# Kernel tuning notes

Hardware: AMD Instinct MI355X
Metric: run time of the kernel (lower is better)

## Reference

```python
import jax, jax.numpy as jnp
import numpy as np

E = 192      # embed_dim
DI = 384     # d_inner = 2*E (mamba default expand=2)
S = 16       # d_state
R = 12       # dt_rank = ceil(E/16)
DEPTH = 4
STRIDE = 4
P = 400      # num_patches = 1600/4
NC = 20
BATCH = 32
EPS = 1e-5


def _rmsnorm(x, w):
    x = x.astype(jnp.float32)
    return x * jax.lax.rsqrt(jnp.mean(x * x, axis=-1, keepdims=True) + EPS) * w


def _mamba_mixer(h, in_w, cw, cb, xpw, dtw, dtb, a_log, d_skip, ow):
    # h: [B, L, E]
    Bsz, Ln, _ = h.shape
    xz = jnp.einsum('ble,de->bld', h, in_w)            # [B,L,2*DI]
    xm, z = xz[..., :DI], xz[..., DI:]
    # causal depthwise conv1d, kernel 4 (left pad 3, truncate to L)
    xp = jnp.pad(xm, ((0, 0), (3, 0), (0, 0)))
    xc = sum(xp[:, k:k + Ln, :] * cw[:, k] for k in range(4)) + cb
    xc = jax.nn.silu(xc)
    xdb = jnp.einsum('bld,rd->blr', xc, xpw)           # [B,L,R+2S]
    dt = jax.nn.softplus(jnp.einsum('blr,dr->bld', xdb[..., :R], dtw) + dtb)
    Bm = xdb[..., R:R + S]
    Cm = xdb[..., R + S:]
    A = -jnp.exp(a_log)                                # [DI,S]

    def step(hst, inp):
        dt_t, b_t, c_t, u_t = inp                      # [B,DI],[B,S],[B,S],[B,DI]
        dA = jnp.exp(dt_t[:, :, None] * A)             # [B,DI,S]
        hst = dA * hst + (dt_t * u_t)[:, :, None] * b_t[:, None, :]
        y_t = jnp.einsum('bdn,bn->bd', hst, c_t)
        return hst, y_t

    h0 = jnp.zeros((Bsz, DI, S), xc.dtype)
    xs = (dt.transpose(1, 0, 2), Bm.transpose(1, 0, 2), Cm.transpose(1, 0, 2), xc.transpose(1, 0, 2))
    _, ys = jax.lax.scan(step, h0, xs)
    y = ys.transpose(1, 0, 2) + xc * d_skip
    y = y * jax.nn.silu(z)
    return jnp.einsum('bld,ed->ble', y, ow)


def _forward(imgs, patch_w, patch_b, cls_token, pos_embed, cnn_w, cnn_b, norm_w,
             in_proj_w, conv_w, conv_b, x_proj_w, dt_proj_w, dt_proj_b, A_log, D,
             out_proj_w, norm_f_w, head_w, head_b):
    Bsz = imgs.shape[0]
    # StrideEmbed: conv1d kernel=stride=4 == reshape + matmul
    x = imgs.reshape(Bsz, P, STRIDE)
    x = jnp.einsum('blk,ek->ble', x, patch_w[:, 0, :]) + patch_b   # [B,P,E]
    x = x + pos_embed[:, :-1, :]
    # depthwise conv1d k=3 pad=1 over length
    xp = jnp.pad(x, ((0, 0), (1, 1), (0, 0)))
    x = sum(xp[:, k:k + P, :] * cnn_w[:, 0, k] for k in range(3)) + cnn_b
    cls = cls_token + pos_embed[:, -1, :]                           # [1,1,E]
    x = jnp.concatenate([x, jnp.broadcast_to(cls, (Bsz, 1, E))], axis=1)  # [B,401,E]

    hidden = x
    residual = None
    for i in range(DEPTH):
        residual = hidden if residual is None else residual + hidden
        hn = _rmsnorm(residual, norm_w[i])
        hidden = _mamba_mixer(hn, in_proj_w[i], conv_w[i], conv_b[i], x_proj_w[i],
                              dt_proj_w[i], dt_proj_b[i], A_log[i], D[i], out_proj_w[i])
    out = _rmsnorm(hidden + residual, norm_f_w)
    v_sem = out[:, -1, :]
    return v_sem @ head_w.T + head_b


def setup_inputs() -> dict:
    key = jax.random.key(0)
    ks = jax.random.split(key, 12)
    n = lambda k, shp, s=0.02: jax.random.normal(k, shp, dtype=jnp.float32) * s
    return {
        'imgs': jax.random.normal(ks[0], (BATCH, 1, 40, 40), jnp.float32),
        'patch_w': n(ks[1], (E, 1, STRIDE), 0.3),
        'patch_b': jnp.zeros((E,), jnp.float32),
        'cls_token': n(ks[2], (1, 1, E)),
        'pos_embed': n(ks[3], (1, P + 1, E)),
        'cnn_w': n(ks[4], (E, 1, 3), 0.3),
        'cnn_b': jnp.zeros((E,), jnp.float32),
        'norm_w': jnp.ones((DEPTH, E), jnp.float32),
        'in_proj_w': n(ks[5], (DEPTH, 2 * DI, E), 0.05),
        'conv_w': n(ks[6], (DEPTH, DI, 4), 0.3),
        'conv_b': jnp.zeros((DEPTH, DI), jnp.float32),
        'x_proj_w': n(ks[7], (DEPTH, R + 2 * S, DI), 0.05),
        'dt_proj_w': n(ks[8], (DEPTH, DI, R), 0.3),
        'dt_proj_b': jnp.log(jnp.expm1(jax.random.uniform(ks[9], (DEPTH, DI), minval=0.001, maxval=0.1))),
        'A_log': jnp.log(jnp.broadcast_to(jnp.arange(1, S + 1, dtype=jnp.float32), (DEPTH, DI, S))),
        'D': jnp.ones((DEPTH, DI), jnp.float32),
        'out_proj_w': n(ks[10], (DEPTH, E, DI), 0.05),
        'norm_f_w': jnp.ones((E,), jnp.float32),
        'head_w': n(ks[11], (NC, E)),
        'head_b': jnp.zeros((NC,), jnp.float32),
    }


def reference(imgs, patch_w, patch_b, cls_token, pos_embed, cnn_w, cnn_b, norm_w,
              in_proj_w, conv_w, conv_b, x_proj_w, dt_proj_w, dt_proj_b, A_log, D,
              out_proj_w, norm_f_w, head_w, head_b):
    return _forward(imgs, patch_w, patch_b, cls_token, pos_embed, cnn_w, cnn_b, norm_w,
                    in_proj_w, conv_w, conv_b, x_proj_w, dt_proj_w, dt_proj_b, A_log, D,
                    out_proj_w, norm_f_w, head_w, head_b)
```

## Files before the change

kernel.cpp:

```cpp
#include <hip/hip_runtime.h>
#include <math.h>

#define E 192
#define DI 384
#define S 16
#define R 12
#define DEPTH 4
#define P 400
#define NC 20
#define BATCH 32
#define L 401
#define NTOK (BATCH * L)
#define CH 32
#define NCH 13

using short8 = __attribute__((ext_vector_type(8))) short;
using float4v = __attribute__((ext_vector_type(4))) float;

__device__ __forceinline__ float siluf(float x) {
    return x / (1.f + __expf(-x));
}
__device__ __forceinline__ float softplusf(float x) {
    return (x > 20.f) ? x : log1pf(__expf(x));
}
__device__ __forceinline__ unsigned short f2bf(float x) {
    unsigned int u = __float_as_uint(x);
    unsigned int r = 0x7fffu + ((u >> 16) & 1u);
    return (unsigned short)((u + r) >> 16);
}

__global__ void k_embed(const float* __restrict__ imgs, const float* __restrict__ patch_w,
                        const float* __restrict__ patch_b, const float* __restrict__ cls_token,
                        const float* __restrict__ pos_embed, const float* __restrict__ cnn_w,
                        const float* __restrict__ cnn_b, float* __restrict__ resid) {
    int idx = blockIdx.x * blockDim.x + threadIdx.x;
    if (idx >= NTOK * E) return;
    int e = idx % E;
    int bl = idx / E;
    int l = bl % L;
    int b = bl / L;
    float out;
    if (l == P) {
        out = cls_token[e] + pos_embed[(size_t)P * E + e];
    } else {
        float w0 = patch_w[e * 4 + 0], w1 = patch_w[e * 4 + 1];
        float w2 = patch_w[e * 4 + 2], w3 = patch_w[e * 4 + 3];
        float pb = patch_b[e];
        const float* ib = imgs + (size_t)b * 1600;
        auto xe = [&](int ll) -> float {
            const float* ip = ib + ll * 4;
            return ip[0] * w0 + ip[1] * w1 + ip[2] * w2 + ip[3] * w3 + pb +
                   pos_embed[(size_t)ll * E + e];
        };
        float c0 = cnn_w[e * 3 + 0], c1 = cnn_w[e * 3 + 1], c2 = cnn_w[e * 3 + 2];
        float acc = cnn_b[e] + xe(l) * c1;
        if (l > 0) acc += xe(l - 1) * c0;
        if (l < P - 1) acc += xe(l + 1) * c2;
        out = acc;
    }
    resid[idx] = out;
}

template <bool ADD>
__global__ void k_rmsnorm(const float* __restrict__ hidden, float* __restrict__ resid,
                          unsigned short* __restrict__ hn, const float* __restrict__ w) {
    int wave = blockIdx.x * (blockDim.x >> 6) + (threadIdx.x >> 6);
    int lane = threadIdx.x & 63;
    if (wave >= NTOK) return;
    size_t base = (size_t)wave * E;
    float v[3];
    float ss = 0.f;
#pragma unroll
    for (int j = 0; j < 3; j++) {
        int e = lane + j * 64;
        float r = resid[base + e];
        if (ADD) {
            r += hidden[base + e];
            resid[base + e] = r;
        }
        v[j] = r;
        ss += r * r;
    }
#pragma unroll
    for (int off = 32; off > 0; off >>= 1) ss += __shfl_xor(ss, off, 64);
    float scale = rsqrtf(ss * (1.f / (float)E) + 1e-5f);
#pragma unroll
    for (int j = 0; j < 3; j++) {
        int e = lane + j * 64;
        hn[base + e] = f2bf(v[j] * scale * w[e]);
    }
}

__global__ void k_cvt(const float* __restrict__ src, unsigned short* __restrict__ dst, int n) {
    int idx = blockIdx.x * blockDim.x + threadIdx.x;
    if (idx < n) dst[idx] = f2bf(src[idx]);
}

__global__ void k_preA(const float* __restrict__ A_log, float* __restrict__ negA, int n) {
    int idx = blockIdx.x * blockDim.x + threadIdx.x;
    if (idx < n) negA[idx] = -__expf(A_log[idx]);
}

template <int BM>
__global__ __launch_bounds__(256) void k_gemm_bf16(const unsigned short* __restrict__ A,
                                                   const unsigned short* __restrict__ W,
                                                   float* __restrict__ C, int M, int N, int K) {
    constexpr int BN = 64, BK = 64, PADK = BK + 8;
    constexpr int MT = BM / 32;
    __shared__ unsigned short As[BM][PADK];
    __shared__ unsigned short Bs[BN][PADK];
    int tid = threadIdx.x;
    int m0 = blockIdx.y * BM, n0 = blockIdx.x * BN;
    int wave = tid >> 6, lane = tid & 63;
    int row16 = lane & 15, quad = lane >> 4;
    int wm0 = (wave >> 1) * (BM / 2), wn0 = (wave & 1) * 32;

    float4v acc[MT][2];
#pragma unroll
    for (int i = 0; i < MT; i++)
#pragma unroll
        for (int j = 0; j < 2; j++) acc[i][j] = (float4v){0.f, 0.f, 0.f, 0.f};

    for (int k0 = 0; k0 < K; k0 += BK) {
#pragma unroll
        for (int p = 0; p < MT; p++) {
            int idx = (p * 256 + tid) * 8;
            int row = idx / BK, col = idx % BK;
            int gm = m0 + row;
            short8 v;
            if (gm < M)
                v = *(const short8*)&A[(size_t)gm * K + k0 + col];
            else
                v = (short8)0;
            *(short8*)&As[row][col] = v;
        }
#pragma unroll
        for (int p = 0; p < 2; p++) {
            int idx = (p * 256 + tid) * 8;
            int row = idx / BK, col = idx % BK;
            int gn = n0 + row;
            short8 v;
            if (gn < N)
                v = *(const short8*)&W[(size_t)gn * K + k0 + col];
            else
                v = (short8)0;
            *(short8*)&Bs[row][col] = v;
        }
        __syncthreads();
#pragma unroll
        for (int kk = 0; kk < BK; kk += 32) {
            int koff = kk + quad * 8;
            short8 af[MT], bfr[2];
#pragma unroll
            for (int i = 0; i < MT; i++)
                af[i] = *(const short8*)&As[wm0 + i * 16 + row16][koff];
#pragma unroll
            for (int j = 0; j < 2; j++)
                bfr[j] = *(const short8*)&Bs[wn0 + j * 16 + row16][koff];
#pragma unroll
            for (int i = 0; i < MT; i++)
#pragma unroll
                for (int j = 0; j < 2; j++)
                    acc[i][j] = __builtin_amdgcn_mfma_f32_16x16x32_bf16(af[i], bfr[j],
                                                                        acc[i][j], 0, 0, 0);
        }
        __syncthreads();
    }
#pragma unroll
    for (int i = 0; i < MT; i++) {
#pragma unroll
        for (int j = 0; j < 2; j++) {
#pragma unroll
            for (int r = 0; r < 4; r++) {
                int m = m0 + wm0 + i * 16 + quad * 4 + r;
                int n = n0 + wn0 + j * 16 + row16;
                if (m < M && n < N) C[(size_t)m * N + n] = acc[i][j][r];
            }
        }
    }
}

__global__ void k_conv(const float* __restrict__ xz, const float* __restrict__ cw,
                       const float* __restrict__ cb, float* __restrict__ xc,
                       unsigned short* __restrict__ xc_bf) {
    int idx = blockIdx.x * blockDim.x + threadIdx.x;
    if (idx >= NTOK * DI) return;
    int d = idx % DI;
    int bl = idx / DI;
    int l = bl % L;
    int b = bl / L;
    const float* base = xz + (size_t)b * L * (2 * DI) + d;
    float acc = cb[d];
#pragma unroll
    for (int k = 0; k < 4; k++) {
        int ll = l - 3 + k;
        if (ll >= 0) acc += base[(size_t)ll * (2 * DI)] * cw[d * 4 + k];
    }
    float v = siluf(acc);
    xc[idx] = v;
    xc_bf[idx] = f2bf(v);
}

__global__ void k_scanA(const float* __restrict__ xc, const float* __restrict__ xdb,
                        const float* __restrict__ negA, const float* __restrict__ dtw,
                        const float* __restrict__ dtb, const float* __restrict__ Dskip,
                        float* __restrict__ ylocal, float* __restrict__ dtcum,
                        float* __restrict__ hend) {
    int d = threadIdx.x;
    int ch = blockIdx.x;
    int b = blockIdx.y;
    int t0 = ch * CH;
    int t1 = min(t0 + CH, L);
    float a[S];
#pragma unroll
    for (int n = 0; n < S; n++) a[n] = negA[d * S + n];
    float wdt[R];
#pragma unroll
    for (int r = 0; r < R; r++) wdt[r] = dtw[d * R + r];
    float bias = dtb[d];
    float dsk = Dskip[d];
    float h[S] = {};
    float dts = 0.f;
    for (int t = t0; t < t1; t++) {
        size_t tok = (size_t)b * L + t;
        const float* row = xdb + tok * 44;
        float dtacc = bias;
#pragma unroll
        for (int r = 0; r < R; r++) dtacc += row[r] * wdt[r];
        float dtv = softplusf(dtacc);
        dts += dtv;
        float u = xc[tok * DI + d];
        float dtu = dtv * u;
        float y = u * dsk;
#pragma unroll
        for (int n = 0; n < S; n++) {
            float dA = __expf(dtv * a[n]);
            h[n] = dA * h[n] + dtu * row[R + n];
            y += h[n] * row[R + S + n];
        }
        ylocal[tok * DI + d] = y;
        dtcum[tok * DI + d] = dts;
    }
    size_t o = (((size_t)b * NCH + ch) * DI + d) * S;
#pragma unroll
    for (int n = 0; n < S; n++) hend[o + n] = h[n];
}

__global__ void k_scanB(const float* __restrict__ hend, const float* __restrict__ dtcum,
                        const float* __restrict__ negA, float* __restrict__ hinit) {
    int idx = blockIdx.x * blockDim.x + threadIdx.x;
    if (idx >= BATCH * DI) return;
    int d = idx % DI;
    int b = idx / DI;
    float a[S];
#pragma unroll
    for (int n = 0; n < S; n++) a[n] = negA[d * S + n];
    float h[S] = {};
    for (int ch = 0; ch < NCH; ch++) {
        size_t o = (((size_t)b * NCH + ch) * DI + d) * S;
#pragma unroll
        for (int n = 0; n < S; n++) hinit[o + n] = h[n];
        int tlast = min(ch * CH + CH, L) - 1;
        float dts = dtcum[((size_t)b * L + tlast) * DI + d];
#pragma unroll
        for (int n = 0; n < S; n++) h[n] = __expf(dts * a[n]) * h[n] + hend[o + n];
    }
}

__global__ void k_fixup(const float* __restrict__ xz, const float* __restrict__ xdb,
                        const float* __restrict__ negA, const float* __restrict__ hinit,
                        const float* __restrict__ ylocal, const float* __restrict__ dtcum,
                        unsigned short* __restrict__ y_bf) {
    int idx = blockIdx.x * blockDim.x + threadIdx.x;
    if (idx >= NTOK * DI) return;
    int d = idx % DI;
    int tok = idx / DI;
    int l = tok % L;
    int b = tok / L;
    int ch = l / CH;
    float y = ylocal[idx];
    if (ch != 0) {
        float dts = dtcum[idx];
        const float* h0 = hinit + (((size_t)b * NCH + ch) * DI + d) * S;
        const float* an = negA + d * S;
        const float* cv = xdb + (size_t)tok * 44 + R + S;
        float corr = 0.f;
#pragma unroll
        for (int n = 0; n < S; n++) corr += cv[n] * __expf(an[n] * dts) * h0[n];
        y += corr;
    }
    float z = xz[(size_t)tok * (2 * DI) + DI + d];
    y_bf[idx] = f2bf(y * siluf(z));
}

__global__ void k_head(const float* __restrict__ resid, const float* __restrict__ hidden,
                       const float* __restrict__ norm_f_w, const float* __restrict__ head_w,
                       const float* __restrict__ head_b, float* __restrict__ out) {
    __shared__ float v[E];
    int b = blockIdx.x;
    int lane = threadIdx.x;
    size_t base = ((size_t)b * L + P) * E;
    float loc[3];
    float ss = 0.f;
#pragma unroll
    for (int j = 0; j < 3; j++) {
        int e = lane + j * 64;
        float x = resid[base + e] + hidden[base + e];
        loc[j] = x;
        ss += x * x;
    }
#pragma unroll
    for (int off = 32; off > 0; off >>= 1) ss += __shfl_xor(ss, off, 64);
    float scale = rsqrtf(ss * (1.f / (float)E) + 1e-5f);
#pragma unroll
    for (int j = 0; j < 3; j++) {
        int e = lane + j * 64;
        v[e] = loc[j] * scale * norm_f_w[e];
    }
    __syncthreads();
    if (lane < NC) {
        float acc = head_b[lane];
        for (int e = 0; e < E; e++) acc += v[e] * head_w[lane * E + e];
        out[b * NC + lane] = acc;
    }
}

extern "C" void kernel_launch(void* const* d_in, const int* in_sizes, int n_in,
                              void* d_out, int out_size, void* d_ws, size_t ws_size,
                              hipStream_t stream) {
    const float* imgs      = (const float*)d_in[0];
    const float* patch_w   = (const float*)d_in[1];
    const float* patch_b   = (const float*)d_in[2];
    const float* cls_token = (const float*)d_in[3];
    const float* pos_embed = (const float*)d_in[4];
    const float* cnn_w     = (const float*)d_in[5];
    const float* cnn_b     = (const float*)d_in[6];
    const float* norm_w    = (const float*)d_in[7];
    const float* in_proj_w = (const float*)d_in[8];
    const float* conv_w    = (const float*)d_in[9];
    const float* conv_b    = (const float*)d_in[10];
    const float* x_proj_w  = (const float*)d_in[11];
    const float* dt_proj_w = (const float*)d_in[12];
    const float* dt_proj_b = (const float*)d_in[13];
    const float* A_log     = (const float*)d_in[14];
    const float* Dskip     = (const float*)d_in[15];
    const float* out_proj_w= (const float*)d_in[16];
    const float* norm_f_w  = (const float*)d_in[17];
    const float* head_w    = (const float*)d_in[18];
    const float* head_b    = (const float*)d_in[19];

    float* ws = (float*)d_ws;
    size_t off = 0;
    float* resid  = ws + off; off += (size_t)NTOK * E;
    float* hidden = ws + off; off += (size_t)NTOK * E;
    float* xz     = ws + off; off += (size_t)NTOK * 2 * DI;
    float* xc     = ws + off; off += (size_t)NTOK * DI;
    float* xdb    = ws + off; off += (size_t)NTOK * 44;
    float* ylocal = ws + off; off += (size_t)NTOK * DI;
    float* dtcum  = ws + off; off += (size_t)NTOK * DI;
    float* hend   = ws + off; off += (size_t)BATCH * NCH * DI * S;
    float* hinit  = ws + off; off += (size_t)BATCH * NCH * DI * S;
    float* negA   = ws + off; off += (size_t)DEPTH * DI * S;
    unsigned short* bf_buf = (unsigned short*)(ws + off); off += (size_t)NTOK * DI / 2;
    unsigned short* w_in  = (unsigned short*)(ws + off); off += (size_t)DEPTH * 2 * DI * E / 2;
    unsigned short* w_x   = (unsigned short*)(ws + off); off += (size_t)DEPTH * 44 * DI / 2 + 16;
    unsigned short* w_out = (unsigned short*)(ws + off); off += (size_t)DEPTH * E * DI / 2;

    unsigned short* hn_bf = bf_buf;
    unsigned short* xc_bf = bf_buf;
    unsigned short* y_bf  = bf_buf;

    {
        int n1 = DEPTH * 2 * DI * E;
        k_cvt<<<(n1 + 255) / 256, 256, 0, stream>>>(in_proj_w, w_in, n1);
        int n2 = DEPTH * 44 * DI;
        k_cvt<<<(n2 + 255) / 256, 256, 0, stream>>>(x_proj_w, w_x, n2);
        int n3 = DEPTH * E * DI;
        k_cvt<<<(n3 + 255) / 256, 256, 0, stream>>>(out_proj_w, w_out, n3);
        int n4 = DEPTH * DI * S;
        k_preA<<<(n4 + 255) / 256, 256, 0, stream>>>(A_log, negA, n4);
    }

    k_embed<<<(NTOK * E) / 256, 256, 0, stream>>>(imgs, patch_w, patch_b, cls_token,
                                                  pos_embed, cnn_w, cnn_b, resid);

    for (int i = 0; i < DEPTH; i++) {
        if (i == 0)
            k_rmsnorm<false><<<NTOK / 4, 256, 0, stream>>>(hidden, resid, hn_bf, norm_w + i * E);
        else
            k_rmsnorm<true><<<NTOK / 4, 256, 0, stream>>>(hidden, resid, hn_bf, norm_w + i * E);

        {
            dim3 g((2 * DI) / 64, (NTOK + 127) / 128);
            k_gemm_bf16<128><<<g, 256, 0, stream>>>(hn_bf, w_in + (size_t)i * 2 * DI * E, xz,
                                                    NTOK, 2 * DI, E);
        }
        k_conv<<<(NTOK * DI) / 256, 256, 0, stream>>>(xz, conv_w + (size_t)i * DI * 4,
                                                      conv_b + (size_t)i * DI, xc, xc_bf);
        {
            dim3 g(1, NTOK / 32);
            k_gemm_bf16<32><<<g, 256, 0, stream>>>(xc_bf, w_x + (size_t)i * 44 * DI, xdb,
                                                   NTOK, 44, DI);
        }
        {
            const float* nA = negA + (size_t)i * DI * S;
            dim3 g(NCH, BATCH);
            k_scanA<<<g, DI, 0, stream>>>(xc, xdb, nA, dt_proj_w + (size_t)i * DI * R,
                                          dt_proj_b + (size_t)i * DI, Dskip + (size_t)i * DI,
                                          ylocal, dtcum, hend);
            k_scanB<<<(BATCH * DI + 255) / 256, 256, 0, stream>>>(hend, dtcum, nA, hinit);
            k_fixup<<<(NTOK * DI + 255) / 256, 256, 0, stream>>>(xz, xdb, nA, hinit,
                                                                 ylocal, dtcum, y_bf);
        }
        {
            dim3 g(E / 64, (NTOK + 63) / 64);
            k_gemm_bf16<64><<<g, 256, 0, stream>>>(y_bf, w_out + (size_t)i * E * DI, hidden,
                                                   NTOK, E, DI);
        }
    }

    k_head<<<BATCH, 64, 0, stream>>>(resid, hidden, norm_f_w, head_w, head_b, (float*)d_out);
}
```

Before: 877.4 us.

## Split scan state across thread pairs, halve chunk size, retile GEMMs, fuse prep kernels

The chunked selective scan now gives each (d) channel two threads, each owning half of the 16 state entries. The two halves of y are combined with a lane shuffle, and the chunk length drops from 32 to 16, which doubles the number of chunks. The GEMM template gains a BN parameter: the in_proj GEMM uses 128x128 tiles and the out_proj GEMM uses 128x64 tiles. The four weight-prep launches are merged into one kernel. The scan changes aim to raise parallelism and shorten the serial dependency chain, at the cost of redundant dt computation per thread pair and larger hend/hinit buffers plus more scanB serial work.

```diff
diff --git a/kernel.cpp b/kernel.cpp
--- a/kernel.cpp
+++ b/kernel.cpp
@@ -11,8 +11,8 @@
 #define BATCH 32
 #define L 401
 #define NTOK (BATCH * L)
-#define CH 32
-#define NCH 13
+#define CH 16
+#define NCH 26
 
 using short8 = __attribute__((ext_vector_type(8))) short;
 using float4v = __attribute__((ext_vector_type(4))) float;
@@ -91,35 +91,48 @@
     }
 }
 
-__global__ void k_cvt(const float* __restrict__ src, unsigned short* __restrict__ dst, int n) {
+__global__ void k_prep(const float* __restrict__ in_proj_w, const float* __restrict__ x_proj_w,
+                       const float* __restrict__ out_proj_w, const float* __restrict__ A_log,
+                       unsigned short* __restrict__ w_in, unsigned short* __restrict__ w_x,
+                       unsigned short* __restrict__ w_out, float* __restrict__ negA) {
+    const int n1 = DEPTH * 2 * DI * E;
+    const int n2 = DEPTH * 44 * DI;
+    const int n3 = DEPTH * E * DI;
+    const int n4 = DEPTH * DI * S;
     int idx = blockIdx.x * blockDim.x + threadIdx.x;
-    if (idx < n) dst[idx] = f2bf(src[idx]);
-}
-
-__global__ void k_preA(const float* __restrict__ A_log, float* __restrict__ negA, int n) {
-    int idx = blockIdx.x * blockDim.x + threadIdx.x;
-    if (idx < n) negA[idx] = -__expf(A_log[idx]);
-}
-
-template <int BM>
+    if (idx < n1) {
+        w_in[idx] = f2bf(in_proj_w[idx]);
+    } else if (idx < n1 + n2) {
+        int i = idx - n1;
+        w_x[i] = f2bf(x_proj_w[i]);
+    } else if (idx < n1 + n2 + n3) {
+        int i = idx - n1 - n2;
+        w_out[i] = f2bf(out_proj_w[i]);
+    } else if (idx < n1 + n2 + n3 + n4) {
+        int i = idx - n1 - n2 - n3;
+        negA[i] = -__expf(A_log[i]);
+    }
+}
+
+template <int BM, int BN>
 __global__ __launch_bounds__(256) void k_gemm_bf16(const unsigned short* __restrict__ A,
                                                    const unsigned short* __restrict__ W,
                                                    float* __restrict__ C, int M, int N, int K) {
-    constexpr int BN = 64, BK = 64, PADK = BK + 8;
-    constexpr int MT = BM / 32;
+    constexpr int BK = 64, PADK = BK + 8;
+    constexpr int MT = BM / 32, NT = BN / 32;
     __shared__ unsigned short As[BM][PADK];
     __shared__ unsigned short Bs[BN][PADK];
     int tid = threadIdx.x;
     int m0 = blockIdx.y * BM, n0 = blockIdx.x * BN;
     int wave = tid >> 6, lane = tid & 63;
     int row16 = lane & 15, quad = lane >> 4;
-    int wm0 = (wave >> 1) * (BM / 2), wn0 = (wave & 1) * 32;
-
-    float4v acc[MT][2];
+    int wm0 = (wave >> 1) * (BM / 2), wn0 = (wave & 1) * (BN / 2);
+
+    float4v acc[MT][NT];
 #pragma unroll
     for (int i = 0; i < MT; i++)
 #pragma unroll
-        for (int j = 0; j < 2; j++) acc[i][j] = (float4v){0.f, 0.f, 0.f, 0.f};
+        for (int j = 0; j < NT; j++) acc[i][j] = (float4v){0.f, 0.f, 0.f, 0.f};
 
     for (int k0 = 0; k0 < K; k0 += BK) {
 #pragma unroll
@@ -135,7 +148,7 @@
             *(short8*)&As[row][col] = v;
         }
 #pragma unroll
-        for (int p = 0; p < 2; p++) {
+        for (int p = 0; p < NT; p++) {
             int idx = (p * 256 + tid) * 8;
             int row = idx / BK, col = idx % BK;
             int gn = n0 + row;
@@ -150,17 +163,17 @@
 #pragma unroll
         for (int kk = 0; kk < BK; kk += 32) {
             int koff = kk + quad * 8;
-            short8 af[MT], bfr[2];
+            short8 af[MT], bfr[NT];
 #pragma unroll
             for (int i = 0; i < MT; i++)
                 af[i] = *(const short8*)&As[wm0 + i * 16 + row16][koff];
 #pragma unroll
-            for (int j = 0; j < 2; j++)
+            for (int j = 0; j < NT; j++)
                 bfr[j] = *(const short8*)&Bs[wn0 + j * 16 + row16][koff];
 #pragma unroll
             for (int i = 0; i < MT; i++)
 #pragma unroll
-                for (int j = 0; j < 2; j++)
+                for (int j = 0; j < NT; j++)
                     acc[i][j] = __builtin_amdgcn_mfma_f32_16x16x32_bf16(af[i], bfr[j],
                                                                         acc[i][j], 0, 0, 0);
         }
@@ -169,7 +182,7 @@
 #pragma unroll
     for (int i = 0; i < MT; i++) {
 #pragma unroll
-        for (int j = 0; j < 2; j++) {
+        for (int j = 0; j < NT; j++) {
 #pragma unroll
             for (int r = 0; r < 4; r++) {
                 int m = m0 + wm0 + i * 16 + quad * 4 + r;
@@ -201,28 +214,31 @@
     xc_bf[idx] = f2bf(v);
 }
 
-__global__ void k_scanA(const float* __restrict__ xc, const float* __restrict__ xdb,
-                        const float* __restrict__ negA, const float* __restrict__ dtw,
-                        const float* __restrict__ dtb, const float* __restrict__ Dskip,
-                        float* __restrict__ ylocal, float* __restrict__ dtcum,
-                        float* __restrict__ hend) {
-    int d = threadIdx.x;
+__global__ __launch_bounds__(768) void k_scanA(
+        const float* __restrict__ xc, const float* __restrict__ xdb,
+        const float* __restrict__ negA, const float* __restrict__ dtw,
+        const float* __restrict__ dtb, const float* __restrict__ Dskip,
+        float* __restrict__ ylocal, float* __restrict__ dtcum,
+        float* __restrict__ hend) {
+    int t = threadIdx.x;
+    int d = t >> 1;
+    int nh = t & 1;
     int ch = blockIdx.x;
     int b = blockIdx.y;
     int t0 = ch * CH;
     int t1 = min(t0 + CH, L);
-    float a[S];
-#pragma unroll
-    for (int n = 0; n < S; n++) a[n] = negA[d * S + n];
+    float a[8];
+#pragma unroll
+    for (int j = 0; j < 8; j++) a[j] = negA[d * S + nh * 8 + j];
     float wdt[R];
 #pragma unroll
     for (int r = 0; r < R; r++) wdt[r] = dtw[d * R + r];
     float bias = dtb[d];
     float dsk = Dskip[d];
-    float h[S] = {};
+    float h[8] = {};
     float dts = 0.f;
-    for (int t = t0; t < t1; t++) {
-        size_t tok = (size_t)b * L + t;
+    for (int tt = t0; tt < t1; tt++) {
+        size_t tok = (size_t)b * L + tt;
         const float* row = xdb + tok * 44;
         float dtacc = bias;
 #pragma unroll
@@ -231,19 +247,22 @@
         dts += dtv;
         float u = xc[tok * DI + d];
         float dtu = dtv * u;
-        float y = u * dsk;
-#pragma unroll
-        for (int n = 0; n < S; n++) {
-            float dA = __expf(dtv * a[n]);
-            h[n] = dA * h[n] + dtu * row[R + n];
-            y += h[n] * row[R + S + n];
-        }
-        ylocal[tok * DI + d] = y;
-        dtcum[tok * DI + d] = dts;
-    }
-    size_t o = (((size_t)b * NCH + ch) * DI + d) * S;
-#pragma unroll
-    for (int n = 0; n < S; n++) hend[o + n] = h[n];
+        float y = nh ? 0.f : u * dsk;
+#pragma unroll
+        for (int j = 0; j < 8; j++) {
+            float dA = __expf(dtv * a[j]);
+            h[j] = dA * h[j] + dtu * row[R + nh * 8 + j];
+            y += h[j] * row[R + S + nh * 8 + j];
+        }
+        y += __shfl_xor(y, 1, 64);
+        if (nh == 0) {
+            ylocal[tok * DI + d] = y;
+            dtcum[tok * DI + d] = dts;
+        }
+    }
+    size_t o = (((size_t)b * NCH + ch) * DI + d) * S + nh * 8;
+#pragma unroll
+    for (int j = 0; j < 8; j++) hend[o + j] = h[j];
 }
 
 __global__ void k_scanB(const float* __restrict__ hend, const float* __restrict__ dtcum,
@@ -371,14 +390,9 @@
     unsigned short* y_bf  = bf_buf;
 
     {
-        int n1 = DEPTH * 2 * DI * E;
-        k_cvt<<<(n1 + 255) / 256, 256, 0, stream>>>(in_proj_w, w_in, n1);
-        int n2 = DEPTH * 44 * DI;
-        k_cvt<<<(n2 + 255) / 256, 256, 0, stream>>>(x_proj_w, w_x, n2);
-        int n3 = DEPTH * E * DI;
-        k_cvt<<<(n3 + 255) / 256, 256, 0, stream>>>(out_proj_w, w_out, n3);
-        int n4 = DEPTH * DI * S;
-        k_preA<<<(n4 + 255) / 256, 256, 0, stream>>>(A_log, negA, n4);
+        int ntot = DEPTH * (2 * DI * E + 44 * DI + E * DI + DI * S);
+        k_prep<<<(ntot + 255) / 256, 256, 0, stream>>>(in_proj_w, x_proj_w, out_proj_w, A_log,
+                                                       w_in, w_x, w_out, negA);
     }
 
     k_embed<<<(NTOK * E) / 256, 256, 0, stream>>>(imgs, patch_w, patch_b, cls_token,
@@ -391,31 +405,31 @@
             k_rmsnorm<true><<<NTOK / 4, 256, 0, stream>>>(hidden, resid, hn_bf, norm_w + i * E);
 
         {
-            dim3 g((2 * DI) / 64, (NTOK + 127) / 128);
-            k_gemm_bf16<128><<<g, 256, 0, stream>>>(hn_bf, w_in + (size_t)i * 2 * DI * E, xz,
-                                                    NTOK, 2 * DI, E);
+            dim3 g((2 * DI) / 128, (NTOK + 127) / 128);
+            k_gemm_bf16<128, 128><<<g, 256, 0, stream>>>(hn_bf, w_in + (size_t)i * 2 * DI * E,
+                                                         xz, NTOK, 2 * DI, E);
         }
         k_conv<<<(NTOK * DI) / 256, 256, 0, stream>>>(xz, conv_w + (size_t)i * DI * 4,
                                                       conv_b + (size_t)i * DI, xc, xc_bf);
         {
             dim3 g(1, NTOK / 32);
-            k_gemm_bf16<32><<<g, 256, 0, stream>>>(xc_bf, w_x + (size_t)i * 44 * DI, xdb,
-                                                   NTOK, 44, DI);
+            k_gemm_bf16<32, 64><<<g, 256, 0, stream>>>(xc_bf, w_x + (size_t)i * 44 * DI, xdb,
+                                                       NTOK, 44, DI);
         }
         {
             const float* nA = negA + (size_t)i * DI * S;
             dim3 g(NCH, BATCH);
-            k_scanA<<<g, DI, 0, stream>>>(xc, xdb, nA, dt_proj_w + (size_t)i * DI * R,
-                                          dt_proj_b + (size_t)i * DI, Dskip + (size_t)i * DI,
-                                          ylocal, dtcum, hend);
+            k_scanA<<<g, 2 * DI, 0, stream>>>(xc, xdb, nA, dt_proj_w + (size_t)i * DI * R,
+                                              dt_proj_b + (size_t)i * DI,
+                                              Dskip + (size_t)i * DI, ylocal, dtcum, hend);
             k_scanB<<<(BATCH * DI + 255) / 256, 256, 0, stream>>>(hend, dtcum, nA, hinit);
             k_fixup<<<(NTOK * DI + 255) / 256, 256, 0, stream>>>(xz, xdb, nA, hinit,
                                                                  ylocal, dtcum, y_bf);
         }
         {
-            dim3 g(E / 64, (NTOK + 63) / 64);
-            k_gemm_bf16<64><<<g, 256, 0, stream>>>(y_bf, w_out + (size_t)i * E * DI, hidden,
-                                                   NTOK, E, DI);
+            dim3 g(E / 64, (NTOK + 127) / 128);
+            k_gemm_bf16<128, 64><<<g, 256, 0, stream>>>(y_bf, w_out + (size_t)i * E * DI,
+                                                        hidden, NTOK, E, DI);
         }
     }
 
```

Result: slower. 983.5 us (+12.1%).
